# Kernel tuning notes

Measured on AMD Instinct MI355X. Metric: run time of the kernel, lower is better.

## Reference

```python
import jax, jax.numpy as jnp
import numpy as np

WS = 8  # window size

def _rel_pos_index(ws):
    coords = np.stack(np.meshgrid(np.arange(ws), np.arange(ws), indexing='ij'))  # (2,ws,ws)
    cf = coords.reshape(2, -1)
    rel = (cf[:, :, None] - cf[:, None, :]).transpose(1, 2, 0).astype(np.int64)
    rel[..., 0] += ws - 1
    rel[..., 1] += ws - 1
    rel[..., 0] *= 2 * ws - 1
    return rel.sum(-1)  # (ws*ws, ws*ws)

REL_IDX = jnp.asarray(_rel_pos_index(WS).reshape(-1))

def _layernorm(x, g, b, eps=1e-5):
    m = x.mean(-1, keepdims=True)
    v = x.var(-1, keepdims=True)
    return (x - m) / jnp.sqrt(v + eps) * g + b

def setup_inputs() -> dict:
    key = jax.random.key(0)
    ks = jax.random.split(key, 32)
    B, Cw, Cs, H, W = 8, 64, 64, 128, 128
    dim, nH, hid = 256, 8, 1024
    n_bias = (2 * WS - 1) * (2 * WS - 1)
    s = 0.02
    d = {}
    d['LH'] = jax.random.normal(ks[0], (B, Cw, H, W), jnp.float32)
    d['HL'] = jax.random.normal(ks[1], (B, Cw, H, W), jnp.float32)
    d['HH'] = jax.random.normal(ks[2], (B, Cw, H, W), jnp.float32)
    d['Spat'] = jax.random.normal(ks[3], (B, Cs, H, W), jnp.float32)
    d['w_hllh'] = jax.random.normal(ks[4], (dim, 2 * Cw), jnp.float32) * s
    d['b_hllh'] = jnp.zeros((dim,), jnp.float32)
    d['w_hh'] = jax.random.normal(ks[5], (dim, Cw), jnp.float32) * s
    d['b_hh'] = jnp.zeros((dim,), jnp.float32)
    d['w_spat'] = jax.random.normal(ks[6], (dim, Cs), jnp.float32) * s
    d['b_spat'] = jnp.zeros((dim,), jnp.float32)
    d['ln1x_g'] = jnp.ones((dim,), jnp.float32)
    d['ln1x_b'] = jnp.zeros((dim,), jnp.float32)
    d['ln1y_g'] = jnp.ones((dim,), jnp.float32)
    d['ln1y_b'] = jnp.zeros((dim,), jnp.float32)
    d['qkv_w'] = jax.random.normal(ks[7], (dim, dim), jnp.float32) * s
    d['qkv_b'] = jnp.zeros((dim,), jnp.float32)
    d['qkv2_w'] = jax.random.normal(ks[8], (dim, dim), jnp.float32) * s
    d['qkv2_b'] = jnp.zeros((dim,), jnp.float32)
    d['qkv3_w'] = jax.random.normal(ks[9], (dim, dim), jnp.float32) * s
    d['qkv3_b'] = jnp.zeros((dim,), jnp.float32)
    d['proj_w'] = jax.random.normal(ks[10], (dim, dim), jnp.float32) * s
    d['proj_b'] = jnp.zeros((dim,), jnp.float32)
    d['rpb_table'] = jax.random.normal(ks[11], (n_bias, nH), jnp.float32) * s
    d['ln2_g'] = jnp.ones((dim,), jnp.float32)
    d['ln2_b'] = jnp.zeros((dim,), jnp.float32)
    d['fc1_w'] = jax.random.normal(ks[12], (hid, dim), jnp.float32) * s
    d['fc1_b'] = jnp.zeros((hid,), jnp.float32)
    d['fc2_w'] = jax.random.normal(ks[13], (dim, hid), jnp.float32) * s
    d['fc2_b'] = jnp.zeros((dim,), jnp.float32)
    return d

def _fwd(LH, HL, HH, Spat, w_hllh, b_hllh, w_hh, b_hh, w_spat, b_spat,
         ln1x_g, ln1x_b, ln1y_g, ln1y_b, qkv_w, qkv_b, qkv2_w, qkv2_b,
         qkv3_w, qkv3_b, proj_w, proj_b, rpb_table, ln2_g, ln2_b,
         fc1_w, fc1_b, fc2_w, fc2_b):
    B, _, H, W = LH.shape
    C = w_hllh.shape[0]
    nH = rpb_table.shape[1]
    hd = C // nH
    N = WS * WS
    # 1x1 convs to common dim, NHWC
    x = jnp.einsum('bchw,oc->bhwo', jnp.concatenate([LH, HL], axis=1), w_hllh) + b_hllh
    z0 = jnp.einsum('bchw,oc->bhwo', HH, w_hh) + b_hh
    y = jnp.einsum('bchw,oc->bhwo', Spat, w_spat) + b_spat
    shortcut = z0.reshape(B, H * W, C)
    xn = _layernorm(x, ln1x_g, ln1x_b)
    yn = _layernorm(y, ln1y_g, ln1y_b)
    # window partition (H,W divisible by WS)
    def part(t):
        t = t.reshape(B, H // WS, WS, W // WS, WS, C).transpose(0, 1, 3, 2, 4, 5)
        return t.reshape(-1, N, C)
    xw = part(xn)
    yw = part(yn)
    zw = yw  # original code: z = F.pad(y, ...) -> value stream is normalized y
    def heads(t, Wm, bm):
        return (t @ Wm.T + bm).reshape(-1, N, nH, hd).transpose(0, 2, 1, 3)
    q = heads(xw, qkv_w, qkv_b) * (hd ** -0.5)
    k = heads(yw, qkv2_w, qkv2_b)
    v = heads(zw, qkv3_w, qkv3_b)
    attn = jnp.einsum('bhnd,bhmd->bhnm', q, k)
    rpb = rpb_table[REL_IDX].reshape(N, N, nH).transpose(2, 0, 1)  # (nH,N,N)
    attn = jax.nn.softmax(attn + rpb[None], axis=-1)
    out = jnp.einsum('bhnm,bhmd->bnhd', attn, v).reshape(-1, N, C)
    out = out @ proj_w.T + proj_b
    # window reverse
    out = out.reshape(B, H // WS, W // WS, WS, WS, C).transpose(0, 1, 3, 2, 4, 5).reshape(B, H * W, C)
    zt = shortcut + out
    h = _layernorm(zt, ln2_g, ln2_b)
    h = jax.nn.gelu(h @ fc1_w.T + fc1_b, approximate=False) @ fc2_w.T + fc2_b
    zt = zt + h
    return zt.reshape(B, H, W, C).transpose(0, 3, 1, 2)

def reference(LH, HL, HH, Spat, w_hllh, b_hllh, w_hh, b_hh, w_spat, b_spat,
              ln1x_g, ln1x_b, ln1y_g, ln1y_b, qkv_w, qkv_b, qkv2_w, qkv2_b,
              qkv3_w, qkv3_b, proj_w, proj_b, rpb_table, ln2_g, ln2_b,
              fc1_w, fc1_b, fc2_w, fc2_b):
    return _fwd(LH, HL, HH, Spat, w_hllh, b_hllh, w_hh, b_hh, w_spat, b_spat,
                ln1x_g, ln1x_b, ln1y_g, ln1y_b, qkv_w, qkv_b, qkv2_w, qkv2_b,
                qkv3_w, qkv3_b, proj_w, proj_b, rpb_table, ln2_g, ln2_b,
                fc1_w, fc1_b, fc2_w, fc2_b)
```

## Files before the change

### kernel.cpp

```cpp
#include <hip/hip_runtime.h>
#include <math.h>

#define DI static __device__ __forceinline__

typedef __attribute__((ext_vector_type(8))) short bhalf8;
typedef __attribute__((ext_vector_type(4))) float floatx4;

DI unsigned short f2bf(float f){
  union { float f; unsigned u; } v; v.f = f;
  unsigned r = (v.u + 0x7fffu + ((v.u >> 16) & 1u)) >> 16;
  return (unsigned short)r;
}
DI float bflo(unsigned v){ return __uint_as_float(v << 16); }
DI float bfhi(unsigned v){ return __uint_as_float(v & 0xffff0000u); }
DI unsigned pk2(float a, float b){ return (unsigned)f2bf(a) | ((unsigned)f2bf(b) << 16); }
DI void unpack8(uint4 u, float* a){
  a[0]=bflo(u.x); a[1]=bfhi(u.x); a[2]=bflo(u.y); a[3]=bfhi(u.y);
  a[4]=bflo(u.z); a[5]=bfhi(u.z); a[6]=bflo(u.w); a[7]=bfhi(u.w);
}
DI float fc(float4 v, int j){ return j==0 ? v.x : (j==1 ? v.y : (j==2 ? v.z : v.w)); }
DI float gelu(float x){
  float u = x*(0.7978845608f + 0.0356774081f*x*x);
  float e = __expf(2.f*u);
  return x - x/(e + 1.f);
}

__global__ void k_scale_vec(const float* __restrict__ src, float* __restrict__ dst, int n, float s){
  int i = blockIdx.x*256 + threadIdx.x;
  if (i < n) dst[i] = src[i]*s;
}
__global__ void k_fragw(const float* __restrict__ src, unsigned short* __restrict__ dst,
                        int n, int K, float scale){
  int t = blockIdx.x*256 + threadIdx.x;
  if (t >= n) return;
  int j = t & 7, lane = (t >> 3) & 63, rest = t >> 9;
  int KS = K >> 5;
  int ks = rest % KS, nt = rest / KS;
  int row = nt*16 + (lane & 15);
  int col = ks*32 + ((lane >> 4) << 3) + j;
  dst[t] = f2bf(src[(size_t)row*K + col] * scale);
}
__global__ void k_bias(const float* __restrict__ rpb, float* __restrict__ biasf){
  int t = blockIdx.x*256 + threadIdx.x;
  int r = t & 3, lane = (t>>2) & 63, nt = (t>>8) & 3, mt = (t>>10) & 3, h = t>>12;
  int qtok = mt*16 + (lane>>4)*4 + r;
  int ktok = nt*16 + (lane & 15);
  int idx = ((qtok>>3) - (ktok>>3) + 7)*15 + ((qtok&7) - (ktok&7) + 7);
  biasf[t] = rpb[idx*8 + h];
}

__global__ __launch_bounds__(256) void k_front(
    const float* __restrict__ LH, const float* __restrict__ HL,
    const float* __restrict__ HH, const float* __restrict__ Sp,
    const unsigned short* __restrict__ wxf, const float* __restrict__ bx,
    const unsigned short* __restrict__ wzf, const float* __restrict__ bz,
    const unsigned short* __restrict__ wyf, const float* __restrict__ by,
    const float* __restrict__ g1x, const float* __restrict__ b1x,
    const float* __restrict__ g1y, const float* __restrict__ b1y,
    const unsigned short* __restrict__ wqf, const float* __restrict__ bq,
    const unsigned short* __restrict__ wkf, const float* __restrict__ bk,
    const unsigned short* __restrict__ wvf, const float* __restrict__ bv,
    unsigned short* __restrict__ z0, unsigned short* __restrict__ qg,
    unsigned short* __restrict__ kg, unsigned short* __restrict__ vtg)
{
  __shared__ __align__(16) unsigned short astg[64*72];
  __shared__ __align__(16) unsigned short sbufA[64*288];
  __shared__ __align__(16) unsigned short sbufB[64*264];
  float* part  = (float*)(sbufA + 16896);
  float* stats = part + 512;

  const int tid = threadIdx.x;
  const int lane = tid & 63, wave = tid >> 6, col = lane & 15, quad = lane >> 4;
  const int mB = blockIdx.x << 6;
  const int b  = mB >> 14;
  const int p0 = mB & 16383;
  const int hrow = p0 >> 7, w0 = p0 & 127;
  const int winb = b*256 + (hrow>>3)*16 + (w0>>3);
  const int tokrow = (hrow & 7)*8;
  const size_t pbase = (size_t)b * (64*16384) + p0;

  float4 f0, f1, f2, f3;
  auto stage_load = [&](const float* plane){
    const float* src = plane + (size_t)((tid>>4)*4)*16384 + (tid&15)*4;
    f0 = *(const float4*)(src);
    f1 = *(const float4*)(src + 16384);
    f2 = *(const float4*)(src + 32768);
    f3 = *(const float4*)(src + 49152);
  };
  auto stage_store = [&](){
    const int tq = tid & 15, c4 = (tid >> 4) * 4;
    #pragma unroll
    for (int j=0;j<4;++j){
      int tok = tq*4 + j;
      int kk = c4 ^ (((tok>>1)&7)<<3);
      uint2 u;
      u.x = pk2(fc(f0,j), fc(f1,j));
      u.y = pk2(fc(f2,j), fc(f3,j));
      *(uint2*)(astg + tok*72 + kk) = u;
    }
  };

  floatx4 c[4][4];
  auto zeroc = [&](){
    #pragma unroll
    for (int mt=0;mt<4;++mt)
      #pragma unroll
      for (int nt=0;nt<4;++nt) c[mt][nt] = (floatx4){0.f,0.f,0.f,0.f};
  };
  auto conv_step = [&](const unsigned short* wf, int KS, int ksg0){
    #pragma unroll
    for (int ksl=0; ksl<2; ++ksl){
      bhalf8 a[4];
      #pragma unroll
      for (int mt=0;mt<4;++mt){
        int tok = mt*16 + col;
        int kk = (ksl*32 + (quad<<3)) ^ (((tok>>1)&7)<<3);
        a[mt] = *(const bhalf8*)(astg + tok*72 + kk);
      }
      #pragma unroll
      for (int nt=0;nt<4;++nt){
        bhalf8 bfr = *(const bhalf8*)(wf + (size_t)(((wave*4+nt)*KS + ksg0 + ksl)*64 + lane)*8);
        #pragma unroll
        for (int mt=0;mt<4;++mt)
          c[mt][nt] = __builtin_amdgcn_mfma_f32_16x16x32_bf16(a[mt], bfr, c[mt][nt], 0, 0, 0);
      }
    }
  };
  auto ln_frag = [&](const float* bias, const float* g, const float* bb2, unsigned short* dst){
    float bv[4];
    #pragma unroll
    for (int nt=0;nt<4;++nt) bv[nt] = bias[wave*64 + nt*16 + col];
    #pragma unroll
    for (int mt=0;mt<4;++mt){
      #pragma unroll
      for (int r=0;r<4;++r){
        float s=0.f, q=0.f;
        #pragma unroll
        for (int nt=0;nt<4;++nt){
          float v = c[mt][nt][r] + bv[nt];
          c[mt][nt][r] = v; s += v; q += v*v;
        }
        s += __shfl_xor(s,1); q += __shfl_xor(q,1);
        s += __shfl_xor(s,2); q += __shfl_xor(q,2);
        s += __shfl_xor(s,4); q += __shfl_xor(q,4);
        s += __shfl_xor(s,8); q += __shfl_xor(q,8);
        if (col == 0){
          int tok = mt*16 + quad*4 + r;
          part[(wave*64+tok)*2+0] = s;
          part[(wave*64+tok)*2+1] = q;
        }
      }
    }
    __syncthreads();
    if (tid < 64){
      float s=0.f, q=0.f;
      #pragma unroll
      for (int w2=0;w2<4;++w2){ s += part[(w2*64+tid)*2]; q += part[(w2*64+tid)*2+1]; }
      float mean = s*(1.f/256.f);
      float var  = q*(1.f/256.f) - mean*mean;
      stats[tid*2]   = mean;
      stats[tid*2+1] = rsqrtf(var + 1e-5f);
    }
    __syncthreads();
    float gv[4], av[4];
    #pragma unroll
    for (int nt=0;nt<4;++nt){ int ch = wave*64+nt*16+col; gv[nt] = g[ch]; av[nt] = bb2[ch]; }
    #pragma unroll
    for (int mt=0;mt<4;++mt)
      #pragma unroll
      for (int r=0;r<4;++r){
        int tok = mt*16 + quad*4 + r;
        float mean = stats[tok*2], rstd = stats[tok*2+1];
        #pragma unroll
        for (int nt=0;nt<4;++nt)
          dst[tok*264 + wave*64 + nt*16 + col] = f2bf((c[mt][nt][r]-mean)*rstd*gv[nt] + av[nt]);
      }
    __syncthreads();
  };

  auto gemm = [&](const unsigned short* Abuf, const unsigned short* wf, const float* bias){
    #pragma unroll
    for (int mt=0;mt<4;++mt)
      #pragma unroll
      for (int nt=0;nt<4;++nt) c[mt][nt] = (floatx4){0.f,0.f,0.f,0.f};
    #pragma unroll
    for (int ks=0; ks<8; ++ks){
      bhalf8 a[4];
      #pragma unroll
      for (int mt=0;mt<4;++mt)
        a[mt] = *(const bhalf8*)(Abuf + (mt*16+col)*264 + ks*32 + (quad<<3));
      #pragma unroll
      for (int nt=0;nt<4;++nt){
        bhalf8 bf = *(const bhalf8*)(wf + (size_t)(((wave*4+nt)*8 + ks)*64 + lane)*8);
        #pragma unroll
        for (int mt=0;mt<4;++mt)
          c[mt][nt] = __builtin_amdgcn_mfma_f32_16x16x32_bf16(a[mt], bf, c[mt][nt], 0, 0, 0);
      }
    }
    #pragma unroll
    for (int nt=0;nt<4;++nt){
      float bb2 = bias[wave*64 + nt*16 + col];
      #pragma unroll
      for (int mt=0;mt<4;++mt)
        #pragma unroll
        for (int r=0;r<4;++r) c[mt][nt][r] += bb2;
    }
  };
  auto stage_write = [&](unsigned short* gout){
    __syncthreads();
    #pragma unroll
    for (int mt=0;mt<4;++mt)
      #pragma unroll
      for (int nt=0;nt<4;++nt)
        #pragma unroll
        for (int r=0;r<4;++r)
          sbufA[(mt*16+quad*4+r)*264 + wave*64 + nt*16 + col] = f2bf(c[mt][nt][r]);
    __syncthreads();
    int tok = tid >> 2, c0 = (tid & 3)*64;
    const uint4* s = (const uint4*)(sbufA + tok*264 + c0);
    uint4* d = (uint4*)(gout + ((size_t)(winb + (tok>>3)))*16384
                             + (size_t)(tokrow + (tok&7))*256 + c0);
    #pragma unroll
    for (int i=0;i<8;++i) d[i] = s[i];
  };

  stage_load(HH + pbase);
  stage_store();
  __syncthreads();
  stage_load(LH + pbase);
  zeroc(); conv_step(wzf, 2, 0);
  {
    #pragma unroll
    for (int nt=0;nt<4;++nt){
      float bzv = bz[wave*64 + nt*16 + col];
      #pragma unroll
      for (int mt=0;mt<4;++mt)
        #pragma unroll
        for (int r=0;r<4;++r) c[mt][nt][r] += bzv;
    }
  }
  stage_write(z0);
  stage_store();
  __syncthreads();
  stage_load(HL + pbase);
  zeroc(); conv_step(wxf, 4, 0);
  __syncthreads();
  stage_store();
  __syncthreads();
  stage_load(Sp + pbase);
  conv_step(wxf, 4, 2);
  __syncthreads();
  stage_store();
  ln_frag(bx, g1x, b1x, sbufA);
  zeroc(); conv_step(wyf, 2, 0);
  ln_frag(by, g1y, b1y, sbufB);
  gemm(sbufA, wqf, bq);
  stage_write(qg);
  gemm(sbufB, wkf, bk);
  stage_write(kg);
  gemm(sbufB, wvf, bv);
  __syncthreads();
  #pragma unroll
  for (int mt=0;mt<4;++mt)
    #pragma unroll
    for (int nt=0;nt<4;++nt){
      int ch = wave*64 + nt*16 + col;
      uint2 u; u.x = pk2(c[mt][nt][0], c[mt][nt][1]); u.y = pk2(c[mt][nt][2], c[mt][nt][3]);
      *(uint2*)(sbufA + ch*72 + mt*16 + quad*4) = u;
    }
  __syncthreads();
  {
    int ch = tid;
    #pragma unroll
    for (int wi=0; wi<8; ++wi){
      uint4 val = *(const uint4*)(sbufA + ch*72 + wi*8);
      *(uint4*)(vtg + ((size_t)(winb + wi))*16384 + ch*64 + tokrow) = val;
    }
  }
}

__global__ __launch_bounds__(256, 2) void k_attnproj(
    const unsigned short* __restrict__ qg, const unsigned short* kg,
    const unsigned short* vtg, const float* __restrict__ biasf,
    const unsigned short* __restrict__ wpf, const float* __restrict__ bp,
    const unsigned short* __restrict__ z0, float* kvf)
{
  __shared__ __align__(16) unsigned short Pb[4*64*72];
  __shared__ __align__(16) unsigned short Ob[64*264];
  const int tid = threadIdx.x, lane = tid & 63, wave = tid >> 6;
  const int col = lane & 15, quad = lane >> 4;
  const int win = blockIdx.x;
  const size_t wbase = (size_t)win * 16384;
  const unsigned short* qw = qg + wbase;
  const unsigned short* kw = kg + wbase;
  const unsigned short* vw = vtg + wbase;
  unsigned short* Pw = Pb + wave*64*72;

  #pragma unroll 1
  for (int hh=0; hh<2; ++hh){
    const int h = wave*2 + hh;
    bhalf8 qf[4], kf[4];
    #pragma unroll
    for (int mt=0;mt<4;++mt)
      qf[mt] = *(const bhalf8*)(qw + (mt*16+col)*256 + h*32 + (quad<<3));
    #pragma unroll
    for (int nt=0;nt<4;++nt)
      kf[nt] = *(const bhalf8*)(kw + (nt*16+col)*256 + h*32 + (quad<<3));
    floatx4 S[4][4];
    #pragma unroll
    for (int mt=0;mt<4;++mt)
      #pragma unroll
      for (int nt=0;nt<4;++nt) S[mt][nt] = (floatx4){0.f,0.f,0.f,0.f};
    #pragma unroll
    for (int mt=0;mt<4;++mt)
      #pragma unroll
      for (int nt=0;nt<4;++nt)
        S[mt][nt] = __builtin_amdgcn_mfma_f32_16x16x32_bf16(qf[mt], kf[nt], S[mt][nt], 0, 0, 0);
    #pragma unroll
    for (int mt=0;mt<4;++mt)
      #pragma unroll
      for (int nt=0;nt<4;++nt){
        float4 bb = *(const float4*)(biasf + (size_t)(((h*4+mt)*4+nt))*256 + lane*4);
        S[mt][nt][0] += bb.x; S[mt][nt][1] += bb.y; S[mt][nt][2] += bb.z; S[mt][nt][3] += bb.w;
      }
    float linv[4][4];
    #pragma unroll
    for (int mt=0;mt<4;++mt){
      #pragma unroll
      for (int r=0;r<4;++r){
        float mx = fmaxf(fmaxf(S[mt][0][r], S[mt][1][r]), fmaxf(S[mt][2][r], S[mt][3][r]));
        mx = fmaxf(mx, __shfl_xor(mx, 1));
        mx = fmaxf(mx, __shfl_xor(mx, 2));
        mx = fmaxf(mx, __shfl_xor(mx, 4));
        mx = fmaxf(mx, __shfl_xor(mx, 8));
        float e0 = __expf(S[mt][0][r]-mx), e1 = __expf(S[mt][1][r]-mx);
        float e2 = __expf(S[mt][2][r]-mx), e3 = __expf(S[mt][3][r]-mx);
        S[mt][0][r]=e0; S[mt][1][r]=e1; S[mt][2][r]=e2; S[mt][3][r]=e3;
        float l = e0+e1+e2+e3;
        l += __shfl_xor(l, 1);
        l += __shfl_xor(l, 2);
        l += __shfl_xor(l, 4);
        l += __shfl_xor(l, 8);
        linv[mt][r] = 1.f/l;
      }
    }
    #pragma unroll
    for (int mt=0;mt<4;++mt)
      #pragma unroll
      for (int nt=0;nt<4;++nt)
        #pragma unroll
        for (int r=0;r<4;++r)
          Pw[(mt*16+quad*4+r)*72 + nt*16 + col] = f2bf(S[mt][nt][r]);
    asm volatile("s_waitcnt lgkmcnt(0)" ::: "memory");
    floatx4 O[4][2];
    #pragma unroll
    for (int mt=0;mt<4;++mt){ O[mt][0]=(floatx4){0.f,0.f,0.f,0.f}; O[mt][1]=(floatx4){0.f,0.f,0.f,0.f}; }
    #pragma unroll
    for (int ks=0; ks<2; ++ks){
      bhalf8 vf[2];
      #pragma unroll
      for (int nt2=0;nt2<2;++nt2)
        vf[nt2] = *(const bhalf8*)(vw + (h*32 + nt2*16 + col)*64 + ks*32 + (quad<<3));
      #pragma unroll
      for (int mt=0;mt<4;++mt){
        bhalf8 pf = *(const bhalf8*)(Pw + (mt*16+col)*72 + ks*32 + (quad<<3));
        #pragma unroll
        for (int nt2=0;nt2<2;++nt2)
          O[mt][nt2] = __builtin_amdgcn_mfma_f32_16x16x32_bf16(pf, vf[nt2], O[mt][nt2], 0, 0, 0);
      }
    }
    #pragma unroll
    for (int mt=0;mt<4;++mt)
      #pragma unroll
      for (int nt2=0;nt2<2;++nt2)
        #pragma unroll
        for (int r=0;r<4;++r)
          Ob[(mt*16+quad*4+r)*264 + h*32 + nt2*16 + col] = f2bf(O[mt][nt2][r]*linv[mt][r]);
  }
  __syncthreads();

  floatx4 c[4][4];
  #pragma unroll
  for (int mt=0;mt<4;++mt)
    #pragma unroll
    for (int nt=0;nt<4;++nt) c[mt][nt] = (floatx4){0.f,0.f,0.f,0.f};
  #pragma unroll
  for (int ks=0; ks<8; ++ks){
    bhalf8 a[4];
    #pragma unroll
    for (int mt=0;mt<4;++mt)
      a[mt] = *(const bhalf8*)(Ob + (mt*16+col)*264 + ks*32 + (quad<<3));
    #pragma unroll
    for (int nt=0;nt<4;++nt){
      bhalf8 bf = *(const bhalf8*)(wpf + (size_t)(((wave*4+nt)*8 + ks)*64 + lane)*8);
      #pragma unroll
      for (int mt=0;mt<4;++mt)
        c[mt][nt] = __builtin_amdgcn_mfma_f32_16x16x32_bf16(a[mt], bf, c[mt][nt], 0, 0, 0);
    }
  }
  float bb[4];
  #pragma unroll
  for (int nt=0;nt<4;++nt) bb[nt] = bp[wave*64 + nt*16 + col];

  float* obuf = (float*)Pb;
  float* ztw  = kvf + (size_t)win * 8192;
  #pragma unroll 1
  for (int p=0; p<2; ++p){
    __syncthreads();
    #pragma unroll
    for (int mt2=0;mt2<2;++mt2){
      int mt = p*2 + mt2;
      #pragma unroll
      for (int nt=0;nt<4;++nt)
        #pragma unroll
        for (int r=0;r<4;++r)
          obuf[(mt2*16+quad*4+r)*260 + wave*64 + nt*16 + col] = c[mt][nt][r] + bb[nt];
    }
    __syncthreads();
    {
      int tl = tid >> 3, c0 = (tid & 7)*32;
      int tok = p*32 + tl;
      const float4* s = (const float4*)(obuf + tl*260 + c0);
      const uint4* zp = (const uint4*)(z0 + ((size_t)win*64 + tok)*256 + c0);
      float zv[32];
      #pragma unroll
      for (int i=0;i<4;++i) unpack8(zp[i], zv + i*8);
      float4* d = (float4*)(ztw + ((tok & 32) ? (size_t)(16777216 + (tok & 31)*256)
                                              : (size_t)tok*256) + c0);
      #pragma unroll
      for (int i=0;i<8;++i){
        float4 o = s[i];
        o.x += zv[i*4+0]; o.y += zv[i*4+1]; o.z += zv[i*4+2]; o.w += zv[i*4+3];
        d[i] = o;
      }
    }
  }
}

__global__ __launch_bounds__(256, 2) void k_mlp(
    const float* __restrict__ kvzt,
    const float* __restrict__ g2, const float* __restrict__ b2,
    const unsigned short* __restrict__ w1f, const float* __restrict__ fc1b,
    const unsigned short* __restrict__ w2f, const float* __restrict__ fc2b,
    float* __restrict__ out)
{
  __shared__ __align__(16) unsigned short smu[2*64*264];
  unsigned short* ztn  = smu;
  unsigned short* hbuf = smu + 64*264;
  float* ob = (float*)smu;

  const int tid  = threadIdx.x;
  const int mB   = blockIdx.x << 6;
  const int lane = tid & 63, wave = tid >> 6;
  const int col  = lane & 15, quad = lane >> 4;

  const int bb_ = mB >> 14;
  const int pp0 = mB & 16383;
  const int hrow = pp0 >> 7, w0 = pp0 & 127;
  const int winb = bb_*256 + (hrow>>3)*16 + (w0>>3);
  const int tokrow = (hrow & 7)*8;
  auto ztoff = [&](int tok)->size_t{
    int wtok = tokrow + (tok & 7);
    size_t o = (size_t)(winb + (tok>>3))*8192;
    o += (wtok & 32) ? (size_t)(16777216 + (wtok & 31)*256) : (size_t)(wtok*256);
    return o;
  };

  {
    const int tok = tid >> 2, qd = tid & 3;
    const float* zr = kvzt + ztoff(tok) + qd*64;
    float v[64];
    #pragma unroll
    for (int j4=0;j4<16;++j4){
      float4 t = ((const float4*)zr)[j4];
      v[j4*4+0]=t.x; v[j4*4+1]=t.y; v[j4*4+2]=t.z; v[j4*4+3]=t.w;
    }
    float s=0.f, q=0.f;
    #pragma unroll
    for (int j=0;j<64;++j){ s += v[j]; q += v[j]*v[j]; }
    s += __shfl_xor(s,1); q += __shfl_xor(q,1);
    s += __shfl_xor(s,2); q += __shfl_xor(q,2);
    float mean = s*(1.f/256.f);
    float rstd = rsqrtf(q*(1.f/256.f) - mean*mean + 1e-5f);
    float gv[64], bv[64];
    #pragma unroll
    for (int j4=0;j4<16;++j4){
      float4 t = ((const float4*)(g2 + qd*64))[j4];
      gv[j4*4+0]=t.x; gv[j4*4+1]=t.y; gv[j4*4+2]=t.z; gv[j4*4+3]=t.w;
      float4 u = ((const float4*)(b2 + qd*64))[j4];
      bv[j4*4+0]=u.x; bv[j4*4+1]=u.y; bv[j4*4+2]=u.z; bv[j4*4+3]=u.w;
    }
    unsigned short* zd = ztn + tok*264 + qd*64;
    #pragma unroll
    for (int j8=0;j8<8;++j8){
      float r[8];
      #pragma unroll
      for (int e=0;e<8;++e) r[e] = (v[j8*8+e]-mean)*rstd*gv[j8*8+e] + bv[j8*8+e];
      uint4 u;
      u.x=pk2(r[0],r[1]); u.y=pk2(r[2],r[3]); u.z=pk2(r[4],r[5]); u.w=pk2(r[6],r[7]);
      *(uint4*)(zd + j8*8) = u;
    }
  }
  __syncthreads();

  floatx4 oacc[4][4];
  #pragma unroll
  for (int i=0;i<4;++i)
    #pragma unroll
    for (int j=0;j<4;++j) oacc[i][j] = (floatx4){0.f,0.f,0.f,0.f};

  #pragma unroll 1
  for (int hb=0; hb<4; ++hb){
    float bv1[4];
    #pragma unroll
    for (int nt=0;nt<4;++nt) bv1[nt] = fc1b[hb*256 + wave*64 + nt*16 + col];
    #pragma unroll 1
    for (int mt=0; mt<4; ++mt){
      floatx4 hacc[4];
      #pragma unroll
      for (int nt=0;nt<4;++nt) hacc[nt] = (floatx4){0.f,0.f,0.f,0.f};
      #pragma unroll
      for (int ks=0; ks<8; ++ks){
        bhalf8 a = *(const bhalf8*)(ztn + (mt*16 + col)*264 + ks*32 + (quad<<3));
        #pragma unroll
        for (int nt=0; nt<4; ++nt){
          int gnt = hb*16 + wave*4 + nt;
          bhalf8 b = *(const bhalf8*)(w1f + (size_t)((gnt*8 + ks)*64 + lane)*8);
          hacc[nt] = __builtin_amdgcn_mfma_f32_16x16x32_bf16(a, b, hacc[nt], 0, 0, 0);
        }
      }
      #pragma unroll
      for (int nt=0; nt<4; ++nt){
        int ch = wave*64 + nt*16 + col;
        #pragma unroll
        for (int r=0;r<4;++r){
          float x = hacc[nt][r] + bv1[nt];
          hbuf[(mt*16 + quad*4 + r)*264 + ch] = f2bf(gelu(x));
        }
      }
    }
    __syncthreads();
    #pragma unroll 1
    for (int mt=0; mt<4; ++mt){
      #pragma unroll
      for (int ks=0; ks<8; ++ks){
        bhalf8 a = *(const bhalf8*)(hbuf + (mt*16 + col)*264 + ks*32 + (quad<<3));
        #pragma unroll
        for (int ot=0; ot<4; ++ot){
          int go = wave*4 + ot;
          bhalf8 b = *(const bhalf8*)(w2f + (size_t)((go*32 + hb*8 + ks)*64 + lane)*8);
          oacc[mt][ot] = __builtin_amdgcn_mfma_f32_16x16x32_bf16(a, b, oacc[mt][ot], 0, 0, 0);
        }
      }
    }
    __syncthreads();
  }

  #pragma unroll
  for (int ot=0; ot<4; ++ot){
    int o = wave*64 + ot*16 + col;
    float bo = fc2b[o];
    #pragma unroll
    for (int mt=0; mt<4; ++mt){
      #pragma unroll
      for (int r=0;r<4;++r){
        int tok = mt*16 + quad*4 + r;
        float zv = kvzt[ztoff(tok) + o];
        ob[tok*257 + o] = oacc[mt][ot][r] + bo + zv;
      }
    }
  }
  __syncthreads();
  {
    const int b = mB >> 14, hw0 = mB & 16383;
    float* obase = out + (size_t)b*(256*16384) + hw0;
    #pragma unroll 1
    for (int it=0; it<64; ++it){
      int l = it*256 + tid;
      int o = l >> 6, tk = l & 63;
      obase[(size_t)o*16384 + tk] = ob[tk*257 + o];
    }
  }
}

extern "C" void kernel_launch(void* const* d_in, const int* in_sizes, int n_in,
                              void* d_out, int out_size, void* d_ws, size_t ws_size,
                              hipStream_t stream)
{
  (void)in_sizes; (void)n_in; (void)out_size; (void)ws_size;
  const float* LH    = (const float*)d_in[0];
  const float* HL    = (const float*)d_in[1];
  const float* HH    = (const float*)d_in[2];
  const float* Spat  = (const float*)d_in[3];
  const float* w_hllh= (const float*)d_in[4];
  const float* b_hllh= (const float*)d_in[5];
  const float* w_hh  = (const float*)d_in[6];
  const float* b_hh  = (const float*)d_in[7];
  const float* w_spat= (const float*)d_in[8];
  const float* b_spat= (const float*)d_in[9];
  const float* ln1x_g= (const float*)d_in[10];
  const float* ln1x_b= (const float*)d_in[11];
  const float* ln1y_g= (const float*)d_in[12];
  const float* ln1y_b= (const float*)d_in[13];
  const float* qkv_w = (const float*)d_in[14];
  const float* qkv_b = (const float*)d_in[15];
  const float* qkv2_w= (const float*)d_in[16];
  const float* qkv2_b= (const float*)d_in[17];
  const float* qkv3_w= (const float*)d_in[18];
  const float* qkv3_b= (const float*)d_in[19];
  const float* proj_w= (const float*)d_in[20];
  const float* proj_b= (const float*)d_in[21];
  const float* rpb   = (const float*)d_in[22];
  const float* ln2_g = (const float*)d_in[23];
  const float* ln2_b = (const float*)d_in[24];
  const float* fc1_w = (const float*)d_in[25];
  const float* fc1_b = (const float*)d_in[26];
  const float* fc2_w = (const float*)d_in[27];
  const float* fc2_b = (const float*)d_in[28];
  float* out = (float*)d_out;

  char* ws = (char*)d_ws;
  size_t off = 0;
  auto alloc = [&](size_t bytes)->void*{
    void* p = ws + off; off += (bytes + 255) & ~(size_t)255; return p;
  };
  const size_t M = 131072;
  unsigned short* z0  = (unsigned short*)alloc(M*256*2);
  unsigned short* qg  = (unsigned short*)alloc(M*256*2);
  char* kv_region     = (char*)alloc(M*256*4);
  unsigned short* kg  = (unsigned short*)kv_region;
  unsigned short* vtg = (unsigned short*)(kv_region + M*256*2);
  float* ztf          = (float*)kv_region;
  unsigned short* wxf = (unsigned short*)alloc(256*128*2);
  unsigned short* wzf = (unsigned short*)alloc(256*64*2);
  unsigned short* wyf = (unsigned short*)alloc(256*64*2);
  unsigned short* wqf = (unsigned short*)alloc(256*256*2);
  unsigned short* wkf = (unsigned short*)alloc(256*256*2);
  unsigned short* wvf = (unsigned short*)alloc(256*256*2);
  unsigned short* wpf = (unsigned short*)alloc(256*256*2);
  unsigned short* w1f = (unsigned short*)alloc(1024*256*2);
  unsigned short* w2f = (unsigned short*)alloc(256*1024*2);
  float* biasf = (float*)alloc(32768*4);
  float* bqs = (float*)alloc(256*4);

  const float sc = 0.17677669529663687f;
  k_fragw<<<dim3(128),  dim3(256), 0, stream>>>(w_hllh, wxf, 256*128, 128, 1.f);
  k_fragw<<<dim3(64),   dim3(256), 0, stream>>>(w_hh,   wzf, 256*64,  64,  1.f);
  k_fragw<<<dim3(64),   dim3(256), 0, stream>>>(w_spat, wyf, 256*64,  64,  1.f);
  k_fragw<<<dim3(256),  dim3(256), 0, stream>>>(qkv_w,  wqf, 256*256, 256, sc);
  k_fragw<<<dim3(256),  dim3(256), 0, stream>>>(qkv2_w, wkf, 256*256, 256, 1.f);
  k_fragw<<<dim3(256),  dim3(256), 0, stream>>>(qkv3_w, wvf, 256*256, 256, 1.f);
  k_fragw<<<dim3(256),  dim3(256), 0, stream>>>(proj_w, wpf, 256*256, 256, 1.f);
  k_fragw<<<dim3(1024), dim3(256), 0, stream>>>(fc1_w,  w1f, 1024*256, 256, 1.f);
  k_fragw<<<dim3(1024), dim3(256), 0, stream>>>(fc2_w,  w2f, 256*1024, 1024, 1.f);
  k_bias <<<dim3(128),  dim3(256), 0, stream>>>(rpb, biasf);
  k_scale_vec<<<dim3(1), dim3(256), 0, stream>>>(qkv_b, bqs, 256, sc);

  k_front<<<dim3(2048), dim3(256), 0, stream>>>(LH, HL, HH, Spat,
      wxf, b_hllh, wzf, b_hh, wyf, b_spat,
      ln1x_g, ln1x_b, ln1y_g, ln1y_b,
      wqf, bqs, wkf, qkv2_b, wvf, qkv3_b,
      z0, qg, kg, vtg);
  k_attnproj<<<dim3(2048), dim3(256), 0, stream>>>(qg, kg, vtg, biasf, wpf, proj_b, z0, ztf);
  k_mlp<<<dim3(2048), dim3(256), 0, stream>>>(ztf, ln2_g, ln2_b,
      w1f, fc1_b, w2f, fc2_b, out);
}
```

Baseline: 1.009 ms.

## Store residual stream as bf16 and shrink MLP hidden buffer for occupancy

The attention-plus-projection kernel now writes the residual result zt as packed bf16 in plain window-major order, reusing the key buffer region, instead of fp32 in a split layout. The MLP kernel reads this bf16 tensor for both the LayerNorm input and the final residual add, which halves the traffic for that intermediate. The MLP hidden activations now go through a double-buffered 16-row tile rather than a full 64-row buffer. The epilogue runs in two 32-token halves, so shared memory per block drops and launch bounds rise to three blocks per CU. The cost is extra rounding in the residual path and more barriers inside the fc1/fc2 loop.

```diff
diff --git a/kernel.cpp b/kernel.cpp
--- a/kernel.cpp
+++ b/kernel.cpp
@@ -283,7 +283,7 @@
     const unsigned short* __restrict__ qg, const unsigned short* kg,
     const unsigned short* vtg, const float* __restrict__ biasf,
     const unsigned short* __restrict__ wpf, const float* __restrict__ bp,
-    const unsigned short* __restrict__ z0, float* kvf)
+    const unsigned short* __restrict__ z0, unsigned short* kvz)
 {
   __shared__ __align__(16) unsigned short Pb[4*64*72];
   __shared__ __align__(16) unsigned short Ob[64*264];
@@ -403,7 +403,7 @@
   for (int nt=0;nt<4;++nt) bb[nt] = bp[wave*64 + nt*16 + col];
 
   float* obuf = (float*)Pb;
-  float* ztw  = kvf + (size_t)win * 8192;
+  unsigned short* ztb = kvz + (size_t)win * 16384;
   #pragma unroll 1
   for (int p=0; p<2; ++p){
     __syncthreads();
@@ -425,28 +425,31 @@
       float zv[32];
       #pragma unroll
       for (int i=0;i<4;++i) unpack8(zp[i], zv + i*8);
-      float4* d = (float4*)(ztw + ((tok & 32) ? (size_t)(16777216 + (tok & 31)*256)
-                                              : (size_t)tok*256) + c0);
-      #pragma unroll
-      for (int i=0;i<8;++i){
-        float4 o = s[i];
-        o.x += zv[i*4+0]; o.y += zv[i*4+1]; o.z += zv[i*4+2]; o.w += zv[i*4+3];
-        d[i] = o;
-      }
-    }
-  }
-}
-
-__global__ __launch_bounds__(256, 2) void k_mlp(
-    const float* __restrict__ kvzt,
+      uint4* d = (uint4*)(ztb + (size_t)tok*256 + c0);
+      #pragma unroll
+      for (int i=0;i<4;++i){
+        float4 a = s[2*i], b4 = s[2*i+1];
+        float r0 = a.x  + zv[i*8+0], r1 = a.y  + zv[i*8+1];
+        float r2 = a.z  + zv[i*8+2], r3 = a.w  + zv[i*8+3];
+        float r4 = b4.x + zv[i*8+4], r5 = b4.y + zv[i*8+5];
+        float r6 = b4.z + zv[i*8+6], r7 = b4.w + zv[i*8+7];
+        uint4 u;
+        u.x = pk2(r0,r1); u.y = pk2(r2,r3); u.z = pk2(r4,r5); u.w = pk2(r6,r7);
+        d[i] = u;
+      }
+    }
+  }
+}
+
+__global__ __launch_bounds__(256, 3) void k_mlp(
+    const unsigned short* __restrict__ kvzt,
     const float* __restrict__ g2, const float* __restrict__ b2,
     const unsigned short* __restrict__ w1f, const float* __restrict__ fc1b,
     const unsigned short* __restrict__ w2f, const float* __restrict__ fc2b,
     float* __restrict__ out)
 {
-  __shared__ __align__(16) unsigned short smu[2*64*264];
-  unsigned short* ztn  = smu;
-  unsigned short* hbuf = smu + 64*264;
+  __shared__ __align__(16) unsigned short smu[96*264];
+  unsigned short* ztn = smu;
   float* ob = (float*)smu;
 
   const int tid  = threadIdx.x;
@@ -459,22 +462,16 @@
   const int hrow = pp0 >> 7, w0 = pp0 & 127;
   const int winb = bb_*256 + (hrow>>3)*16 + (w0>>3);
   const int tokrow = (hrow & 7)*8;
-  auto ztoff = [&](int tok)->size_t{
-    int wtok = tokrow + (tok & 7);
-    size_t o = (size_t)(winb + (tok>>3))*8192;
-    o += (wtok & 32) ? (size_t)(16777216 + (wtok & 31)*256) : (size_t)(wtok*256);
-    return o;
+  auto ztrow = [&](int tok)->size_t{
+    return ((size_t)(winb + (tok>>3))*64 + (size_t)(tokrow + (tok&7))) * 256;
   };
 
   {
     const int tok = tid >> 2, qd = tid & 3;
-    const float* zr = kvzt + ztoff(tok) + qd*64;
+    const uint4* zr = (const uint4*)(kvzt + ztrow(tok) + qd*64);
     float v[64];
     #pragma unroll
-    for (int j4=0;j4<16;++j4){
-      float4 t = ((const float4*)zr)[j4];
-      v[j4*4+0]=t.x; v[j4*4+1]=t.y; v[j4*4+2]=t.z; v[j4*4+3]=t.w;
-    }
+    for (int j=0;j<8;++j) unpack8(zr[j], v + j*8);
     float s=0.f, q=0.f;
     #pragma unroll
     for (int j=0;j<64;++j){ s += v[j]; q += v[j]*v[j]; }
@@ -514,8 +511,9 @@
     float bv1[4];
     #pragma unroll
     for (int nt=0;nt<4;++nt) bv1[nt] = fc1b[hb*256 + wave*64 + nt*16 + col];
-    #pragma unroll 1
+    #pragma unroll
     for (int mt=0; mt<4; ++mt){
+      unsigned short* hb16 = smu + 64*264 + (mt & 1)*16*264;
       floatx4 hacc[4];
       #pragma unroll
       for (int nt=0;nt<4;++nt) hacc[nt] = (floatx4){0.f,0.f,0.f,0.f};
@@ -533,18 +531,13 @@
       for (int nt=0; nt<4; ++nt){
         int ch = wave*64 + nt*16 + col;
         #pragma unroll
-        for (int r=0;r<4;++r){
-          float x = hacc[nt][r] + bv1[nt];
-          hbuf[(mt*16 + quad*4 + r)*264 + ch] = f2bf(gelu(x));
-        }
-      }
-    }
-    __syncthreads();
-    #pragma unroll 1
-    for (int mt=0; mt<4; ++mt){
+        for (int r=0;r<4;++r)
+          hb16[(quad*4 + r)*264 + ch] = f2bf(gelu(hacc[nt][r] + bv1[nt]));
+      }
+      __syncthreads();
       #pragma unroll
       for (int ks=0; ks<8; ++ks){
-        bhalf8 a = *(const bhalf8*)(hbuf + (mt*16 + col)*264 + ks*32 + (quad<<3));
+        bhalf8 a = *(const bhalf8*)(hb16 + col*264 + ks*32 + (quad<<3));
         #pragma unroll
         for (int ot=0; ot<4; ++ot){
           int go = wave*4 + ot;
@@ -553,31 +546,35 @@
         }
       }
     }
-    __syncthreads();
-  }
-
+  }
+
+  float bo[4];
   #pragma unroll
-  for (int ot=0; ot<4; ++ot){
-    int o = wave*64 + ot*16 + col;
-    float bo = fc2b[o];
-    #pragma unroll
-    for (int mt=0; mt<4; ++mt){
-      #pragma unroll
-      for (int r=0;r<4;++r){
-        int tok = mt*16 + quad*4 + r;
-        float zv = kvzt[ztoff(tok) + o];
-        ob[tok*257 + o] = oacc[mt][ot][r] + bo + zv;
-      }
-    }
-  }
-  __syncthreads();
-  {
-    const int b = mB >> 14, hw0 = mB & 16383;
-    float* obase = out + (size_t)b*(256*16384) + hw0;
+  for (int ot=0;ot<4;++ot) bo[ot] = fc2b[wave*64 + ot*16 + col];
+  const int bgl = mB >> 14, hw0 = mB & 16383;
+  #pragma unroll 1
+  for (int p=0; p<2; ++p){
+    __syncthreads();
+    #pragma unroll
+    for (int mt2=0; mt2<2; ++mt2){
+      int mt = p*2 + mt2;
+      #pragma unroll
+      for (int ot=0; ot<4; ++ot){
+        int ch = wave*64 + ot*16 + col;
+        #pragma unroll
+        for (int r=0;r<4;++r){
+          int tok = mt*16 + quad*4 + r;
+          float zv = bflo((unsigned)kvzt[ztrow(tok) + ch]);
+          ob[(mt2*16 + quad*4 + r)*257 + ch] = oacc[mt][ot][r] + bo[ot] + zv;
+        }
+      }
+    }
+    __syncthreads();
+    float* obase = out + (size_t)bgl*(256*16384) + hw0 + p*32;
     #pragma unroll 1
-    for (int it=0; it<64; ++it){
+    for (int it=0; it<32; ++it){
       int l = it*256 + tid;
-      int o = l >> 6, tk = l & 63;
+      int o = l >> 5, tk = l & 31;
       obase[(size_t)o*16384 + tk] = ob[tk*257 + o];
     }
   }
@@ -630,7 +627,7 @@
   char* kv_region     = (char*)alloc(M*256*4);
   unsigned short* kg  = (unsigned short*)kv_region;
   unsigned short* vtg = (unsigned short*)(kv_region + M*256*2);
-  float* ztf          = (float*)kv_region;
+  unsigned short* ztb = (unsigned short*)kv_region;
   unsigned short* wxf = (unsigned short*)alloc(256*128*2);
   unsigned short* wzf = (unsigned short*)alloc(256*64*2);
   unsigned short* wyf = (unsigned short*)alloc(256*64*2);
@@ -661,7 +658,7 @@
       ln1x_g, ln1x_b, ln1y_g, ln1y_b,
       wqf, bqs, wkf, qkv2_b, wvf, qkv3_b,
       z0, qg, kg, vtg);
-  k_attnproj<<<dim3(2048), dim3(256), 0, stream>>>(qg, kg, vtg, biasf, wpf, proj_b, z0, ztf);
-  k_mlp<<<dim3(2048), dim3(256), 0, stream>>>(ztf, ln2_g, ln2_b,
+  k_attnproj<<<dim3(2048), dim3(256), 0, stream>>>(qg, kg, vtg, biasf, wpf, proj_b, z0, ztb);
+  k_mlp<<<dim3(2048), dim3(256), 0, stream>>>(ztb, ln2_g, ln2_b,
       w1f, fc1_b, w2f, fc2_b, out);
 }
```

Measured after the change: 1.535 ms. +52.1%, slower.
